# Performance work log

Hardware: AMD Instinct MI355X
Metric: run time of the kernel (lower is better)

## Reference

```python
import jax, jax.numpy as jnp
import numpy as np

B, T, D_MODEL, D_HEAD = 4, 4096, 512, 64  # batch, token_depth, token_len, d_head
D_K = 64
NEG = -1.0e9  # mask fill value used by the torch module


def setup_inputs() -> dict:
    key = jax.random.key(0)
    kx, kq, kk, kv = jax.random.split(key, 4)
    x = jax.random.normal(kx, (B, T, D_MODEL), dtype=jnp.float32)
    # nn.Linear(token_len, d_head, bias=False) -> weight shape [d_head, token_len]
    Wq = jax.random.normal(kq, (D_HEAD, D_MODEL), dtype=jnp.float32) * 0.02
    Wk = jax.random.normal(kk, (D_HEAD, D_MODEL), dtype=jnp.float32) * 0.02
    Wv = jax.random.normal(kv, (D_HEAD, D_MODEL), dtype=jnp.float32) * 0.02
    return {"x": x, "Wq": Wq, "Wk": Wk, "Wv": Wv}


def reference(x, Wq, Wk, Wv):
    # q/k/v projections: y = x @ W.T  (Linear with bias=False)
    q = jnp.einsum("btd,hd->bth", x, Wq)  # [B,T,D_HEAD]
    k = jnp.einsum("btd,hd->bth", x, Wk)
    v = jnp.einsum("btd,hd->bth", x, Wv)

    scores = jnp.einsum("bth,bsh->bts", q, k)  # [B,T,T]

    # additive causal mask: upper triangle (diagonal=1) filled with -1e9
    t_idx = jnp.arange(T)
    mask = jnp.where(t_idx[None, :] > t_idx[:, None], NEG, 0.0).astype(scores.dtype)
    scores = scores + mask[None, :, :]

    sqrt_dk = jnp.sqrt(jnp.asarray(D_K, dtype=scores.dtype))
    # NOTE: original code applies softmax over dim=1 (the query axis), not -1.
    attn = jax.nn.softmax(scores / sqrt_dk, axis=1)
    out = jnp.einsum("bts,bsh->bth", attn, v)  # [B,T,D_HEAD]
    return out
```

## Files before the change

### kernel.cpp

```cpp
#include <hip/hip_runtime.h>

#define B_ 4
#define T_ 4096
#define DM 512
#define DH 64
#define CS 512
#define CTS 512

typedef short short8 __attribute__((ext_vector_type(8)));
typedef short bf16x4 __attribute__((ext_vector_type(4)));
typedef float f32x4 __attribute__((ext_vector_type(4)));
typedef float float8 __attribute__((ext_vector_type(8)));

__device__ inline short f2bf(float f) {
    unsigned u = __float_as_uint(f);
    u += 0x7fffu + ((u >> 16) & 1u);
    return (short)(u >> 16);
}
__device__ inline float bf2f(short s) {
    return __uint_as_float(((unsigned)(unsigned short)s) << 16);
}
__device__ inline short8 cvt8(const float* p) {
    float8 v = *(const float8*)p;
    short8 r;
#pragma unroll
    for (int j = 0; j < 8; j++) r[j] = f2bf(v[j]);
    return r;
}
__device__ inline unsigned cvt_pk_bf16(float a, float b) {
    unsigned r;
    asm("v_cvt_pk_bf16_f32 %0, %1, %2" : "=v"(r) : "v"(a), "v"(b));
    return r;
}
__device__ inline bf16x4 pmask4(f32x4 d, int sbase, int t) {
    float p[4];
#pragma unroll
    for (int r = 0; r < 4; r++) {
        float e = __expf(d[r] * 0.125f);
        p[r] = (sbase + r <= t) ? e : 0.f;
    }
    union { unsigned u[2]; bf16x4 v; } z;
    z.u[0] = cvt_pk_bf16(p[0], p[1]);
    z.u[1] = cvt_pk_bf16(p[2], p[3]);
    return z.v;
}

__global__ __launch_bounds__(256, 4) void k_proj(
    const float* __restrict__ x, const float* __restrict__ Wq,
    const float* __restrict__ Wk, const float* __restrict__ Wv,
    short* __restrict__ qb, short* __restrict__ kb, short* __restrict__ vb,
    float* __restrict__ lsum)
{
    __shared__ short Xs[16 * 72];
    __shared__ short Ws[192 * 72];
    int tid = threadIdx.x;
    int lane = tid & 63, w = tid >> 6;
    int l16 = lane & 15, quad = lane >> 4;
    int b = blockIdx.x >> 8;
    int tile = blockIdx.x & 255;
    int t0 = tile * 16;
    long xbase = ((long)(b * T_ + t0)) * DM;
    int hb = w * 3;

    if (tid < 16) lsum[blockIdx.x * 16 + tid] = 0.f;

    f32x4 acc[3];
#pragma unroll
    for (int i = 0; i < 3; i++) acc[i] = (f32x4)(0.f);

    for (int kc = 0; kc < DM; kc += 64) {
        if (tid < 128) {
            int row = tid >> 3, col = (tid & 7) * 8;
            *(short8*)(Xs + row * 72 + col) = cvt8(x + xbase + (long)row * DM + kc + col);
        }
#pragma unroll
        for (int p = 0; p < 6; p++) {
            int idx = p * 256 + tid;
            int row = idx >> 3, col = (idx & 7) * 8;
            const float* Wsrc = (p < 2) ? Wq : (p < 4) ? Wk : Wv;
            *(short8*)(Ws + row * 72 + col) = cvt8(Wsrc + (long)(row & 63) * DM + kc + col);
        }
        __syncthreads();
#pragma unroll
        for (int ks = 0; ks < 2; ks++) {
            short8 af = *(const short8*)(Xs + l16 * 72 + ks * 32 + quad * 8);
#pragma unroll
            for (int j = 0; j < 3; j++) {
                short8 bf = *(const short8*)(Ws + ((hb + j) * 16 + l16) * 72 + ks * 32 + quad * 8);
                acc[j] = __builtin_amdgcn_mfma_f32_16x16x32_bf16(af, bf, acc[j], 0, 0, 0);
            }
        }
        __syncthreads();
    }
#pragma unroll
    for (int j = 0; j < 3; j++) {
        int hh = hb + j, m = hh >> 2, h4 = hh & 3;
        short* outp = (m == 0) ? qb : (m == 1) ? kb : vb;
#pragma unroll
        for (int r4 = 0; r4 < 4; r4++) {
            int t = t0 + quad * 4 + r4;
            outp[((long)(b * T_ + t)) * DH + h4 * 16 + l16] = f2bf(acc[j][r4]);
        }
    }
}

__global__ __launch_bounds__(256, 4) void k_stats(
    const short* __restrict__ qb, const short* __restrict__ kb,
    float* __restrict__ lsum, float* __restrict__ out)
{
    __shared__ short Qb[128 * 72];
    int tid = threadIdx.x;
    int lane = tid & 63, w = tid >> 6;
    int l16 = lane & 15, quad = lane >> 4;

    *(f32x4*)(out + ((long)blockIdx.x * 256 + tid) * 4) = (f32x4)(0.f);

    const int NC = T_ / CTS;
    int chunk = blockIdx.x % NC;
    int st = (blockIdx.x / NC) & 31;
    int b = blockIdx.x / (NC * 32);
    int c0 = chunk * CTS, cend = c0 + CTS;
    int s0blk = st * 128;
    if (cend <= s0blk) return;
    int s0w = s0blk + w * 32;
    long bq = (long)b * T_ * DH;

    const short8* kp0 = (const short8*)(kb + bq + (long)(s0w + l16) * DH + quad * 8);
    short8 a00 = kp0[0], a01 = kp0[4];
    const short8* kp1 = (const short8*)(kb + bq + (long)(s0w + 16 + l16) * DH + quad * 8);
    short8 a10 = kp1[0], a11 = kp1[4];

    int t_lo = (c0 > s0blk) ? c0 : s0blk;
    int nsteps = (cend - t_lo) >> 7;
    float acc0[4] = {0.f, 0.f, 0.f, 0.f};
    float acc1[4] = {0.f, 0.f, 0.f, 0.f};

    for (int stp = 0; stp < nsteps; stp++) {
        int t0 = t_lo + stp * 128;
#pragma unroll
        for (int p = 0; p < 4; p++) {
            int idx = p * 256 + tid;
            int row = idx >> 3, col = idx & 7;
            *(short8*)(Qb + row * 72 + col * 8) =
                *(const short8*)(qb + bq + (long)(t0 + row) * DH + col * 8);
        }
        __syncthreads();
        for (int sub = 0; sub < 8; sub++) {
            int tt = t0 + sub * 16;
            if (tt + 15 >= s0w) {
                short8 b0 = *(const short8*)(Qb + (sub * 16 + l16) * 72 + quad * 8);
                short8 b1 = *(const short8*)(Qb + (sub * 16 + l16) * 72 + 32 + quad * 8);
                int t = tt + l16;
                f32x4 d0 = (f32x4)(0.f);
                d0 = __builtin_amdgcn_mfma_f32_16x16x32_bf16(a00, b0, d0, 0, 0, 0);
                d0 = __builtin_amdgcn_mfma_f32_16x16x32_bf16(a01, b1, d0, 0, 0, 0);
#pragma unroll
                for (int r = 0; r < 4; r++) {
                    int s = s0w + quad * 4 + r;
                    float p = __expf(d0[r] * 0.125f);
                    acc0[r] += (t >= s) ? p : 0.f;
                }
                if (tt + 15 >= s0w + 16) {
                    f32x4 d1 = (f32x4)(0.f);
                    d1 = __builtin_amdgcn_mfma_f32_16x16x32_bf16(a10, b0, d1, 0, 0, 0);
                    d1 = __builtin_amdgcn_mfma_f32_16x16x32_bf16(a11, b1, d1, 0, 0, 0);
#pragma unroll
                    for (int r = 0; r < 4; r++) {
                        int s = s0w + 16 + quad * 4 + r;
                        float p = __expf(d1[r] * 0.125f);
                        acc1[r] += (t >= s) ? p : 0.f;
                    }
                }
            }
        }
        __syncthreads();
    }
#pragma unroll
    for (int r = 0; r < 4; r++) {
        float v = acc0[r];
        v += __shfl_xor(v, 1, 16); v += __shfl_xor(v, 2, 16);
        v += __shfl_xor(v, 4, 16); v += __shfl_xor(v, 8, 16);
        if (l16 == 0) atomicAdd(&lsum[b * T_ + s0w + quad * 4 + r], v);
        float v1 = acc1[r];
        v1 += __shfl_xor(v1, 1, 16); v1 += __shfl_xor(v1, 2, 16);
        v1 += __shfl_xor(v1, 4, 16); v1 += __shfl_xor(v1, 8, 16);
        if (l16 == 0) atomicAdd(&lsum[b * T_ + s0w + 16 + quad * 4 + r], v1);
    }
}

__global__ __launch_bounds__(256) void k_vt(
    const short* __restrict__ vb, const float* __restrict__ lsum, short* __restrict__ vTc)
{
    int tid = threadIdx.x;
    int b = blockIdx.x >> 6;
    int s0 = (blockIdx.x & 63) * 64;
    int h = tid & 63, g = tid >> 6;
    long vbase = ((long)(b * T_) + s0 + g * 16) * DH + h;
    long lbase = (long)b * T_ + s0 + g * 16;
    short8 lo, hi;
#pragma unroll
    for (int k2 = 0; k2 < 8; k2++) {
        float rl = 1.0f / lsum[lbase + k2];
        lo[k2] = f2bf(bf2f(vb[vbase + (long)k2 * DH]) * rl);
        float rh = 1.0f / lsum[lbase + 8 + k2];
        hi[k2] = f2bf(bf2f(vb[vbase + (long)(8 + k2) * DH]) * rh);
    }
    long ob = ((long)(b * 256 + (s0 >> 4) + g) * 64 + h) * 16;
    *(short8*)(vTc + ob) = lo;
    *(short8*)(vTc + ob + 8) = hi;
}

__global__ __launch_bounds__(256, 4) void k_out(
    const short* __restrict__ qb, const short* __restrict__ kb,
    const short* __restrict__ vTc, float* __restrict__ out)
{
    __shared__ short Kb[128 * 72];
    int tid = threadIdx.x;
    int lane = tid & 63, w = tid >> 6;
    int l16 = lane & 15, quad = lane >> 4;
    const int NC = T_ / CS;
    int chunk = blockIdx.x % NC;
    int strip = (blockIdx.x / NC) & 31;
    int b = blockIdx.x / (NC * 32);
    int c0 = chunk * CS;
    int blk_tmax = strip * 128 + 127;
    if (c0 > blk_tmax) return;
    int s_hi = (c0 + CS < blk_tmax + 1) ? c0 + CS : blk_tmax + 1;
    int nsteps = (s_hi - c0 + 127) >> 7;
    int t0w = strip * 128 + w * 32;
    long bq = (long)b * T_ * DH;

    const short8* qp0 = (const short8*)(qb + bq + (long)(t0w + l16) * DH + quad * 8);
    short8 q00 = qp0[0], q01 = qp0[4];
    const short8* qp1 = (const short8*)(qb + bq + (long)(t0w + 16 + l16) * DH + quad * 8);
    short8 q10 = qp1[0], q11 = qp1[4];
    const short* vTb = vTc + (long)b * (T_ / 16) * DH * 16;

    f32x4 o0[4], o1[4];
#pragma unroll
    for (int i = 0; i < 4; i++) { o0[i] = (f32x4)(0.f); o1[i] = (f32x4)(0.f); }
    int t0 = t0w + l16, t1 = t0 + 16;

    for (int stp = 0; stp < nsteps; stp++) {
        int s0 = c0 + stp * 128;
#pragma unroll
        for (int p = 0; p < 4; p++) {
            int idx = p * 256 + tid;
            int row = idx >> 3, col = idx & 7;
            *(short8*)(Kb + row * 72 + col * 8) =
                *(const short8*)(kb + bq + (long)(s0 + row) * DH + col * 8);
        }
        __syncthreads();

        for (int sub = 0; sub < 8; sub++) {
            int sc = s0 + sub * 16;
            if (sc > t0w + 31) break;
            short8 a0 = *(const short8*)(Kb + (sub * 16 + l16) * 72 + quad * 8);
            short8 a1 = *(const short8*)(Kb + (sub * 16 + l16) * 72 + 32 + quad * 8);
            const short* vc = vTb + (long)(sc >> 4) * 1024 + quad * 4;
            bf16x4 bv[4];
#pragma unroll
            for (int h4 = 0; h4 < 4; h4++)
                bv[h4] = *(const bf16x4*)(vc + (h4 * 16 + l16) * 16);

            f32x4 d1 = (f32x4)(0.f);
            d1 = __builtin_amdgcn_mfma_f32_16x16x32_bf16(a0, q10, d1, 0, 0, 0);
            d1 = __builtin_amdgcn_mfma_f32_16x16x32_bf16(a1, q11, d1, 0, 0, 0);
            bf16x4 pa1 = pmask4(d1, sc + quad * 4, t1);

            bf16x4 pa0 = (bf16x4)(short)0;
            if (sc <= t0w + 15) {
                f32x4 d0 = (f32x4)(0.f);
                d0 = __builtin_amdgcn_mfma_f32_16x16x32_bf16(a0, q00, d0, 0, 0, 0);
                d0 = __builtin_amdgcn_mfma_f32_16x16x32_bf16(a1, q01, d0, 0, 0, 0);
                pa0 = pmask4(d0, sc + quad * 4, t0);
            }
#pragma unroll
            for (int h4 = 0; h4 < 4; h4++) {
                o1[h4] = __builtin_amdgcn_mfma_f32_16x16x16bf16_1k(pa1, bv[h4], o1[h4], 0, 0, 0);
                o0[h4] = __builtin_amdgcn_mfma_f32_16x16x16bf16_1k(pa0, bv[h4], o0[h4], 0, 0, 0);
            }
        }
        __syncthreads();
    }
#pragma unroll
    for (int h4 = 0; h4 < 4; h4++)
#pragma unroll
        for (int r = 0; r < 4; r++) {
            int t = t0w + quad * 4 + r;
            atomicAdd(&out[bq + (long)t * DH + h4 * 16 + l16], o0[h4][r]);
            atomicAdd(&out[bq + (long)(t + 16) * DH + h4 * 16 + l16], o1[h4][r]);
        }
}

extern "C" void kernel_launch(void* const* d_in, const int* in_sizes, int n_in,
                              void* d_out, int out_size, void* d_ws, size_t ws_size,
                              hipStream_t stream) {
    const float* x  = (const float*)d_in[0];
    const float* Wq = (const float*)d_in[1];
    const float* Wk = (const float*)d_in[2];
    const float* Wv = (const float*)d_in[3];
    float* out = (float*)d_out;

    char* ws = (char*)d_ws;
    short* qb   = (short*)(ws);
    short* kb   = (short*)(ws + (2l << 20));
    short* vb   = (short*)(ws + (4l << 20));
    short* vTc  = (short*)(ws + (6l << 20));
    float* lsum = (float*)(ws + (8l << 20));

    k_proj<<<dim3(B_ * T_ / 16), dim3(256), 0, stream>>>(x, Wq, Wk, Wv, qb, kb, vb, lsum);
    k_stats<<<dim3(B_ * 32 * (T_ / CTS)), dim3(256), 0, stream>>>(qb, kb, lsum, out);
    k_vt<<<dim3(B_ * T_ / 64), dim3(256), 0, stream>>>(vb, lsum, vTc);
    k_out<<<dim3(B_ * 32 * (T_ / CS)), dim3(256), 0, stream>>>(qb, kb, vTc, out);
}
```

Before: 150.9 us.

## Map one block per causal 128x128 tile via triangular index decode

Replaces the chunked grid, where many blocks exit early and others loop over several 128-wide steps, with a grid of exactly the 528 lower-triangular tile pairs per batch. Each block decodes its (i,j) tile from a linear index using a sqrt-based triangular decode and processes a single tile, so no blocks are idle and per-block work is nearly uniform. The stats kernel walks tiles in reverse order so the heavy ones launch first. Occupancy hints rise from 4 to 6 blocks per SIMD. The cost is more atomic adds into lsum and the output, since every tile now adds its partial results separately.

```diff
diff --git a/kernel.cpp b/kernel.cpp
--- a/kernel.cpp
+++ b/kernel.cpp
@@ -4,8 +4,8 @@
 #define T_ 4096
 #define DM 512
 #define DH 64
-#define CS 512
-#define CTS 512
+#define NSTRIP 32
+#define NTRI 528
 
 typedef short short8 __attribute__((ext_vector_type(8)));
 typedef short bf16x4 __attribute__((ext_vector_type(4)));
@@ -43,6 +43,13 @@
     z.u[0] = cvt_pk_bf16(p[0], p[1]);
     z.u[1] = cvt_pk_bf16(p[2], p[3]);
     return z.v;
+}
+__device__ inline void tri_decode(int m, int& i, int& j) {
+    int ii = (int)((__builtin_sqrtf(8.f * (float)m + 1.f) - 1.f) * 0.5f);
+    while ((ii + 1) * (ii + 2) / 2 <= m) ii++;
+    while (ii * (ii + 1) / 2 > m) ii--;
+    i = ii;
+    j = m - ii * (ii + 1) / 2;
 }
 
 __global__ __launch_bounds__(256, 4) void k_proj(
@@ -104,7 +111,7 @@
     }
 }
 
-__global__ __launch_bounds__(256, 4) void k_stats(
+__global__ __launch_bounds__(256, 6) void k_stats(
     const short* __restrict__ qb, const short* __restrict__ kb,
     float* __restrict__ lsum, float* __restrict__ out)
 {
@@ -113,15 +120,15 @@
     int lane = tid & 63, w = tid >> 6;
     int l16 = lane & 15, quad = lane >> 4;
 
-    *(f32x4*)(out + ((long)blockIdx.x * 256 + tid) * 4) = (f32x4)(0.f);
-
-    const int NC = T_ / CTS;
-    int chunk = blockIdx.x % NC;
-    int st = (blockIdx.x / NC) & 31;
-    int b = blockIdx.x / (NC * 32);
-    int c0 = chunk * CTS, cend = c0 + CTS;
-    int s0blk = st * 128;
-    if (cend <= s0blk) return;
+    if (blockIdx.x < 1024)
+        *(f32x4*)(out + ((long)blockIdx.x * 256 + tid) * 4) = (f32x4)(0.f);
+
+    int b = blockIdx.x / NTRI;
+    int m = blockIdx.x - b * NTRI;
+    int ii, jj; tri_decode(NTRI - 1 - m, ii, jj);
+    int i = (NSTRIP - 1) - ii, j = (NSTRIP - 1) - jj;
+    int s0blk = i * 128;
+    int t0 = j * 128;
     int s0w = s0blk + w * 32;
     long bq = (long)b * T_ * DH;
 
@@ -130,50 +137,44 @@
     const short8* kp1 = (const short8*)(kb + bq + (long)(s0w + 16 + l16) * DH + quad * 8);
     short8 a10 = kp1[0], a11 = kp1[4];
 
-    int t_lo = (c0 > s0blk) ? c0 : s0blk;
-    int nsteps = (cend - t_lo) >> 7;
     float acc0[4] = {0.f, 0.f, 0.f, 0.f};
     float acc1[4] = {0.f, 0.f, 0.f, 0.f};
 
-    for (int stp = 0; stp < nsteps; stp++) {
-        int t0 = t_lo + stp * 128;
-#pragma unroll
-        for (int p = 0; p < 4; p++) {
-            int idx = p * 256 + tid;
-            int row = idx >> 3, col = idx & 7;
-            *(short8*)(Qb + row * 72 + col * 8) =
-                *(const short8*)(qb + bq + (long)(t0 + row) * DH + col * 8);
-        }
-        __syncthreads();
-        for (int sub = 0; sub < 8; sub++) {
-            int tt = t0 + sub * 16;
-            if (tt + 15 >= s0w) {
-                short8 b0 = *(const short8*)(Qb + (sub * 16 + l16) * 72 + quad * 8);
-                short8 b1 = *(const short8*)(Qb + (sub * 16 + l16) * 72 + 32 + quad * 8);
-                int t = tt + l16;
-                f32x4 d0 = (f32x4)(0.f);
-                d0 = __builtin_amdgcn_mfma_f32_16x16x32_bf16(a00, b0, d0, 0, 0, 0);
-                d0 = __builtin_amdgcn_mfma_f32_16x16x32_bf16(a01, b1, d0, 0, 0, 0);
+#pragma unroll
+    for (int p = 0; p < 4; p++) {
+        int idx = p * 256 + tid;
+        int row = idx >> 3, col = idx & 7;
+        *(short8*)(Qb + row * 72 + col * 8) =
+            *(const short8*)(qb + bq + (long)(t0 + row) * DH + col * 8);
+    }
+    __syncthreads();
+    for (int sub = 0; sub < 8; sub++) {
+        int tt = t0 + sub * 16;
+        if (tt + 15 >= s0w) {
+            short8 b0 = *(const short8*)(Qb + (sub * 16 + l16) * 72 + quad * 8);
+            short8 b1 = *(const short8*)(Qb + (sub * 16 + l16) * 72 + 32 + quad * 8);
+            int t = tt + l16;
+            f32x4 d0 = (f32x4)(0.f);
+            d0 = __builtin_amdgcn_mfma_f32_16x16x32_bf16(a00, b0, d0, 0, 0, 0);
+            d0 = __builtin_amdgcn_mfma_f32_16x16x32_bf16(a01, b1, d0, 0, 0, 0);
+#pragma unroll
+            for (int r = 0; r < 4; r++) {
+                int s = s0w + quad * 4 + r;
+                float p = __expf(d0[r] * 0.125f);
+                acc0[r] += (t >= s) ? p : 0.f;
+            }
+            if (tt + 15 >= s0w + 16) {
+                f32x4 d1 = (f32x4)(0.f);
+                d1 = __builtin_amdgcn_mfma_f32_16x16x32_bf16(a10, b0, d1, 0, 0, 0);
+                d1 = __builtin_amdgcn_mfma_f32_16x16x32_bf16(a11, b1, d1, 0, 0, 0);
 #pragma unroll
                 for (int r = 0; r < 4; r++) {
-                    int s = s0w + quad * 4 + r;
-                    float p = __expf(d0[r] * 0.125f);
-                    acc0[r] += (t >= s) ? p : 0.f;
-                }
-                if (tt + 15 >= s0w + 16) {
-                    f32x4 d1 = (f32x4)(0.f);
-                    d1 = __builtin_amdgcn_mfma_f32_16x16x32_bf16(a10, b0, d1, 0, 0, 0);
-                    d1 = __builtin_amdgcn_mfma_f32_16x16x32_bf16(a11, b1, d1, 0, 0, 0);
-#pragma unroll
-                    for (int r = 0; r < 4; r++) {
-                        int s = s0w + 16 + quad * 4 + r;
-                        float p = __expf(d1[r] * 0.125f);
-                        acc1[r] += (t >= s) ? p : 0.f;
-                    }
+                    int s = s0w + 16 + quad * 4 + r;
+                    float p = __expf(d1[r] * 0.125f);
+                    acc1[r] += (t >= s) ? p : 0.f;
                 }
             }
         }
-        __syncthreads();
     }
 #pragma unroll
     for (int r = 0; r < 4; r++) {
@@ -210,7 +211,7 @@
     *(short8*)(vTc + ob + 8) = hi;
 }
 
-__global__ __launch_bounds__(256, 4) void k_out(
+__global__ __launch_bounds__(256, 6) void k_out(
     const short* __restrict__ qb, const short* __restrict__ kb,
     const short* __restrict__ vTc, float* __restrict__ out)
 {
@@ -218,16 +219,11 @@
     int tid = threadIdx.x;
     int lane = tid & 63, w = tid >> 6;
     int l16 = lane & 15, quad = lane >> 4;
-    const int NC = T_ / CS;
-    int chunk = blockIdx.x % NC;
-    int strip = (blockIdx.x / NC) & 31;
-    int b = blockIdx.x / (NC * 32);
-    int c0 = chunk * CS;
-    int blk_tmax = strip * 128 + 127;
-    if (c0 > blk_tmax) return;
-    int s_hi = (c0 + CS < blk_tmax + 1) ? c0 + CS : blk_tmax + 1;
-    int nsteps = (s_hi - c0 + 127) >> 7;
-    int t0w = strip * 128 + w * 32;
+    int b = blockIdx.x / NTRI;
+    int m = blockIdx.x - b * NTRI;
+    int i, j; tri_decode(m, i, j);
+    int s0 = j * 128;
+    int t0w = i * 128 + w * 32;
     long bq = (long)b * T_ * DH;
 
     const short8* qp0 = (const short8*)(qb + bq + (long)(t0w + l16) * DH + quad * 8);
@@ -238,51 +234,48 @@
 
     f32x4 o0[4], o1[4];
 #pragma unroll
-    for (int i = 0; i < 4; i++) { o0[i] = (f32x4)(0.f); o1[i] = (f32x4)(0.f); }
+    for (int ii = 0; ii < 4; ii++) { o0[ii] = (f32x4)(0.f); o1[ii] = (f32x4)(0.f); }
     int t0 = t0w + l16, t1 = t0 + 16;
 
-    for (int stp = 0; stp < nsteps; stp++) {
-        int s0 = c0 + stp * 128;
-#pragma unroll
-        for (int p = 0; p < 4; p++) {
-            int idx = p * 256 + tid;
-            int row = idx >> 3, col = idx & 7;
-            *(short8*)(Kb + row * 72 + col * 8) =
-                *(const short8*)(kb + bq + (long)(s0 + row) * DH + col * 8);
-        }
-        __syncthreads();
-
-        for (int sub = 0; sub < 8; sub++) {
-            int sc = s0 + sub * 16;
-            if (sc > t0w + 31) break;
-            short8 a0 = *(const short8*)(Kb + (sub * 16 + l16) * 72 + quad * 8);
-            short8 a1 = *(const short8*)(Kb + (sub * 16 + l16) * 72 + 32 + quad * 8);
-            const short* vc = vTb + (long)(sc >> 4) * 1024 + quad * 4;
-            bf16x4 bv[4];
-#pragma unroll
-            for (int h4 = 0; h4 < 4; h4++)
-                bv[h4] = *(const bf16x4*)(vc + (h4 * 16 + l16) * 16);
-
-            f32x4 d1 = (f32x4)(0.f);
-            d1 = __builtin_amdgcn_mfma_f32_16x16x32_bf16(a0, q10, d1, 0, 0, 0);
-            d1 = __builtin_amdgcn_mfma_f32_16x16x32_bf16(a1, q11, d1, 0, 0, 0);
-            bf16x4 pa1 = pmask4(d1, sc + quad * 4, t1);
-
-            bf16x4 pa0 = (bf16x4)(short)0;
-            if (sc <= t0w + 15) {
-                f32x4 d0 = (f32x4)(0.f);
-                d0 = __builtin_amdgcn_mfma_f32_16x16x32_bf16(a0, q00, d0, 0, 0, 0);
-                d0 = __builtin_amdgcn_mfma_f32_16x16x32_bf16(a1, q01, d0, 0, 0, 0);
-                pa0 = pmask4(d0, sc + quad * 4, t0);
-            }
-#pragma unroll
-            for (int h4 = 0; h4 < 4; h4++) {
-                o1[h4] = __builtin_amdgcn_mfma_f32_16x16x16bf16_1k(pa1, bv[h4], o1[h4], 0, 0, 0);
-                o0[h4] = __builtin_amdgcn_mfma_f32_16x16x16bf16_1k(pa0, bv[h4], o0[h4], 0, 0, 0);
-            }
-        }
-        __syncthreads();
-    }
+#pragma unroll
+    for (int p = 0; p < 4; p++) {
+        int idx = p * 256 + tid;
+        int row = idx >> 3, col = idx & 7;
+        *(short8*)(Kb + row * 72 + col * 8) =
+            *(const short8*)(kb + bq + (long)(s0 + row) * DH + col * 8);
+    }
+    __syncthreads();
+
+    for (int sub = 0; sub < 8; sub++) {
+        int sc = s0 + sub * 16;
+        if (sc > t0w + 31) break;
+        short8 a0 = *(const short8*)(Kb + (sub * 16 + l16) * 72 + quad * 8);
+        short8 a1 = *(const short8*)(Kb + (sub * 16 + l16) * 72 + 32 + quad * 8);
+        const short* vc = vTb + (long)(sc >> 4) * 1024 + quad * 4;
+        bf16x4 bv[4];
+#pragma unroll
+        for (int h4 = 0; h4 < 4; h4++)
+            bv[h4] = *(const bf16x4*)(vc + (h4 * 16 + l16) * 16);
+
+        f32x4 d1 = (f32x4)(0.f);
+        d1 = __builtin_amdgcn_mfma_f32_16x16x32_bf16(a0, q10, d1, 0, 0, 0);
+        d1 = __builtin_amdgcn_mfma_f32_16x16x32_bf16(a1, q11, d1, 0, 0, 0);
+        bf16x4 pa1 = pmask4(d1, sc + quad * 4, t1);
+
+        bf16x4 pa0 = (bf16x4)(short)0;
+        if (sc <= t0w + 15) {
+            f32x4 d0 = (f32x4)(0.f);
+            d0 = __builtin_amdgcn_mfma_f32_16x16x32_bf16(a0, q00, d0, 0, 0, 0);
+            d0 = __builtin_amdgcn_mfma_f32_16x16x32_bf16(a1, q01, d0, 0, 0, 0);
+            pa0 = pmask4(d0, sc + quad * 4, t0);
+        }
+#pragma unroll
+        for (int h4 = 0; h4 < 4; h4++) {
+            o1[h4] = __builtin_amdgcn_mfma_f32_16x16x16bf16_1k(pa1, bv[h4], o1[h4], 0, 0, 0);
+            o0[h4] = __builtin_amdgcn_mfma_f32_16x16x16bf16_1k(pa0, bv[h4], o0[h4], 0, 0, 0);
+        }
+    }
+
 #pragma unroll
     for (int h4 = 0; h4 < 4; h4++)
 #pragma unroll
@@ -310,7 +303,7 @@
     float* lsum = (float*)(ws + (8l << 20));
 
     k_proj<<<dim3(B_ * T_ / 16), dim3(256), 0, stream>>>(x, Wq, Wk, Wv, qb, kb, vb, lsum);
-    k_stats<<<dim3(B_ * 32 * (T_ / CTS)), dim3(256), 0, stream>>>(qb, kb, lsum, out);
+    k_stats<<<dim3(B_ * NTRI), dim3(256), 0, stream>>>(qb, kb, lsum, out);
     k_vt<<<dim3(B_ * T_ / 64), dim3(256), 0, stream>>>(vb, lsum, vTc);
-    k_out<<<dim3(B_ * 32 * (T_ / CS)), dim3(256), 0, stream>>>(qb, kb, vTc, out);
-}
+    k_out<<<dim3(B_ * NTRI), dim3(256), 0, stream>>>(qb, kb, vTc, out);
+}
```

After: 176.7 us. 17.1% more time.
